# Kernel tuning notes

Measured on AMD Instinct MI355X. Metric: run time of the kernel, lower is better.

Reference implementation:

```python
import jax, jax.numpy as jnp
import numpy as np
import math

E = 8        # num_experts
L2 = 15
L3 = 32
D = 3072     # eval_features_per_perspective
R = 256      # router_features
B = 16384
AUX_ALPHA = 0.01
Z_ALPHA = 0.001


def setup_inputs() -> dict:
    key = jax.random.key(0)
    ks = jax.random.split(key, 12)
    inp = {
        "expert_input": jax.random.uniform(ks[0], (B, D), jnp.float32),
        "router_input": jax.random.normal(ks[1], (R,) , jnp.float32) * 0 + jax.random.normal(ks[1], (B, R), jnp.float32),
        # router init: normal(std=0.01), zero bias (as in _reset_router)
        "router_w": jax.random.normal(ks[2], (E, R), jnp.float32) * 0.01,
        "router_b": jnp.zeros((E,), jnp.float32),
        # FactorizedStackedLinear l1: stacked weight [E*(L2+1), D] + shared factorized [(L2+1), D]
        "l1_w": jax.random.normal(ks[3], (E * (L2 + 1), D), jnp.float32) * (1.0 / math.sqrt(D)),
        "l1_b": jax.random.normal(ks[4], (E * (L2 + 1),), jnp.float32) * 0.01,
        "l1f_w": jax.random.normal(ks[5], (L2 + 1, D), jnp.float32) * (1.0 / math.sqrt(D)),
        "l1f_b": jax.random.normal(ks[6], (L2 + 1,), jnp.float32) * 0.01,
        # StackedLinear l2: [E*L3, 2*L2]
        "l2_w": jax.random.normal(ks[7], (E * L3, 2 * L2), jnp.float32) * (1.0 / math.sqrt(2 * L2)),
        "l2_b": jax.random.normal(ks[8], (E * L3,), jnp.float32) * 0.01,
        # StackedLinear output: [E*1, L3], bias zeroed in __init__
        "out_w": jax.random.normal(ks[9], (E, L3), jnp.float32) * (1.0 / math.sqrt(L3)),
        "out_b": jnp.zeros((E,), jnp.float32),
    }
    return inp


def reference(expert_input, router_input, router_w, router_b,
              l1_w, l1_b, l1f_w, l1f_b, l2_w, l2_b, out_w, out_b):
    # ---- router + straight-through hard gate ----
    gate_logits = router_input @ router_w.T + router_b                      # [B, E]
    gate_probs = jax.nn.softmax(gate_logits, axis=-1)
    expert_indices = jnp.argmax(gate_logits, axis=-1)                       # [B]
    hard_gate = jax.nn.one_hot(expert_indices, E, dtype=gate_probs.dtype)   # [B, E]
    gate = hard_gate + gate_probs - jax.lax.stop_gradient(gate_probs)

    # ---- routing metrics / losses ----
    fraction_routed = hard_gate.mean(axis=0)                                 # [E]
    avg_gate_prob = gate_probs.mean(axis=0)                                  # [E]
    aux_loss = E * jnp.sum(fraction_routed * avg_gate_prob)
    z_loss = jnp.mean(jnp.square(jax.nn.logsumexp(gate_logits, axis=-1)))
    entropy = jnp.mean(-jnp.sum(gate_probs * jnp.log(jnp.clip(gate_probs, 1e-9)), axis=-1))
    normalized_entropy = entropy / jnp.float32(math.log(max(E, 2)))
    top1_prob = jnp.mean(jnp.max(gate_probs, axis=-1))
    router_loss = jnp.float32(AUX_ALPHA) * aux_loss + jnp.float32(Z_ALPHA) * z_loss  # training path

    # ---- l1: FactorizedStackedLinear, dense over all experts (training path) ----
    merged_w = (l1_w + jnp.tile(l1f_w, (E, 1))).reshape(E, L2 + 1, D)        # [E, L2+1, D]
    merged_b = (l1_b + jnp.tile(l1f_b, (E,))).reshape(E, L2 + 1)             # [E, L2+1]
    l1c = jnp.einsum('bi,eoi->beo', expert_input, merged_w) + merged_b[None]  # [B, E, L2+1]
    l1x, l1x_out = l1c[:, :, :L2], l1c[:, :, L2:]                            # [B,E,L2], [B,E,1]
    l1x = jnp.clip(jnp.concatenate([jnp.square(l1x) * (255.0 / 256.0), l1x], axis=2), 0.0, 1.0)  # [B,E,2*L2]

    # ---- l2 + output StackedLinear ----
    w2 = l2_w.reshape(E, L3, 2 * L2)
    l2x = jnp.clip(jnp.einsum('bei,eoi->beo', l1x, w2) + l2_b.reshape(E, L3)[None], 0.0, 1.0)  # [B,E,L3]
    wo = out_w.reshape(E, 1, L3)
    l3x = jnp.einsum('bei,eoi->beo', l2x, wo) + out_b.reshape(E, 1)[None] + l1x_out            # [B,E,1]

    # ---- gated combine ----
    out = jnp.einsum('be,beo->bo', gate, l3x)                                # [B, 1]
    return (out, router_loss, aux_loss, z_loss, fraction_routed, avg_gate_prob,
            normalized_entropy, top1_prob)
```

## Files before the change

kernel.cpp:

```cpp
#include <hip/hip_runtime.h>

constexpr int NB  = 16384;
constexpr int ND  = 3072;
constexpr int NR  = 256;
constexpr int NE  = 8;
constexpr int NO1 = 16;
constexpr int NL2D = 30;
constexpr int NL3 = 32;

constexpr size_t WS_CURSORS = 32;
constexpr size_t WS_OFFPAD  = 128;
constexpr size_t WS_IDX     = 256;
constexpr size_t WS_BUCKET  = WS_IDX + (size_t)NB*4;
constexpr size_t WS_MB      = WS_BUCKET + (size_t)(NB+256)*4;
constexpr size_t WS_MW      = WS_MB + 512;
constexpr size_t WS_BLK_CNT  = WS_MW + (size_t)128*3072*4;
constexpr size_t WS_BLK_SUMP = WS_BLK_CNT + 8192;
constexpr size_t WS_BLK_Z    = WS_BLK_SUMP + 8192;
constexpr size_t WS_BLK_ENT  = WS_BLK_Z + 1024;
constexpr size_t WS_BLK_TOP  = WS_BLK_ENT + 1024;

__device__ __forceinline__ float clamp01(float v) { return fminf(fmaxf(v, 0.0f), 1.0f); }

__device__ __forceinline__ void stage16(const float* g, float* l) {
    __builtin_amdgcn_global_load_lds(
        (const __attribute__((address_space(1))) unsigned int*)g,
        (__attribute__((address_space(3))) unsigned int*)l,
        16, 0, 0);
}

__global__ __launch_bounds__(256) void router_merge_kernel(
    const float* __restrict__ rin, const float* __restrict__ rw,
    const float* __restrict__ rb, int* __restrict__ idx,
    int* __restrict__ blk_cnt, float* __restrict__ blk_sump,
    float* __restrict__ blk_z, float* __restrict__ blk_ent, float* __restrict__ blk_top,
    const float* __restrict__ l1w, const float* __restrict__ l1b,
    const float* __restrict__ l1fw, const float* __restrict__ l1fb,
    float* __restrict__ mw, float* __restrict__ mb)
{
    const int t = threadIdx.x;

    if (blockIdx.x >= 256) {
        const int gid = blockIdx.x - 256;
        const int i4 = gid * 256 + t;
        const float4 a = ((const float4*)l1w)[i4];
        const float4 b = ((const float4*)l1fw)[i4 % (NO1 * ND / 4)];
        float4 r; r.x = a.x + b.x; r.y = a.y + b.y; r.z = a.z + b.z; r.w = a.w + b.w;
        ((float4*)mw)[i4] = r;
        if (gid == 0 && t < NE * NO1) {
            mb[t] = l1b[t] + l1fb[t & (NO1 - 1)];
        }
        return;
    }

    __shared__ float w_s[NE][NR];
    __shared__ float red_f[4][11];
    __shared__ int   red_c[4][8];

    {
        const float4* src = (const float4*)rw;
        float4* dst = (float4*)&w_s[0][0];
        dst[t]       = src[t];
        dst[t + 256] = src[t + 256];
    }
    __syncthreads();

    const int q  = t & 3;
    const int rr = t >> 2;
    const int b  = blockIdx.x * 64 + rr;
    const float* rp = rin + (size_t)b * NR + q * 64;

    float acc[NE];
#pragma unroll
    for (int e = 0; e < NE; ++e) acc[e] = 0.0f;

#pragma unroll
    for (int c = 0; c < 16; ++c) {
        const float4 xv = *(const float4*)(rp + c * 4);
#pragma unroll
        for (int e = 0; e < NE; ++e) {
            const float4 wv = *(const float4*)(&w_s[e][q * 64 + c * 4]);
            acc[e] = fmaf(xv.x, wv.x, acc[e]);
            acc[e] = fmaf(xv.y, wv.y, acc[e]);
            acc[e] = fmaf(xv.z, wv.z, acc[e]);
            acc[e] = fmaf(xv.w, wv.w, acc[e]);
        }
    }
    float lg[NE];
#pragma unroll
    for (int e = 0; e < NE; ++e) {
        float v = acc[e];
        v += __shfl_xor(v, 1);
        v += __shfl_xor(v, 2);
        lg[e] = v + rb[e];
    }

    float m = lg[0]; int am = 0;
#pragma unroll
    for (int e = 1; e < NE; ++e) { if (lg[e] > m) { m = lg[e]; am = e; } }
    float p[NE]; float ssum = 0.0f;
#pragma unroll
    for (int e = 0; e < NE; ++e) { p[e] = __expf(lg[e] - m); ssum += p[e]; }
    const float inv = 1.0f / ssum;
    const float lse = m + __logf(ssum);

    const bool active = (q == 0);
    float sv[11];
    float ent = 0.0f, top = 0.0f;
#pragma unroll
    for (int e = 0; e < NE; ++e) {
        const float pj = p[e] * inv;
        sv[e] = pj;
        ent -= pj * __logf(fmaxf(pj, 1e-9f));
        top = fmaxf(top, pj);
    }
    sv[8] = lse * lse;
    sv[9] = ent;
    sv[10] = top;
    if (!active) {
#pragma unroll
        for (int i = 0; i < 11; ++i) sv[i] = 0.0f;
    }
    if (active) idx[b] = am;

#pragma unroll
    for (int i = 0; i < 11; ++i) {
        float v = sv[i];
        v += __shfl_xor(v, 4);
        v += __shfl_xor(v, 8);
        v += __shfl_xor(v, 16);
        v += __shfl_xor(v, 32);
        sv[i] = v;
    }
    int cnt[NE];
#pragma unroll
    for (int j = 0; j < NE; ++j) {
        unsigned long long mk = __ballot(active && (am == j));
        cnt[j] = __popcll(mk);
    }

    const int wave = t >> 6;
    if ((t & 63) == 0) {
#pragma unroll
        for (int i = 0; i < 11; ++i) red_f[wave][i] = sv[i];
#pragma unroll
        for (int j = 0; j < NE; ++j) red_c[wave][j] = cnt[j];
    }
    __syncthreads();

    const int bid = blockIdx.x;
    if (t < 8) {
        blk_sump[bid * 8 + t] = red_f[0][t] + red_f[1][t] + red_f[2][t] + red_f[3][t];
        blk_cnt [bid * 8 + t] = red_c[0][t] + red_c[1][t] + red_c[2][t] + red_c[3][t];
    } else if (t == 8) {
        blk_z[bid]   = red_f[0][8] + red_f[1][8] + red_f[2][8] + red_f[3][8];
    } else if (t == 9) {
        blk_ent[bid] = red_f[0][9] + red_f[1][9] + red_f[2][9] + red_f[3][9];
    } else if (t == 10) {
        blk_top[bid] = red_f[0][10] + red_f[1][10] + red_f[2][10] + red_f[3][10];
    }
}

__global__ __launch_bounds__(256) void scatter_finalize_kernel(
    const int* __restrict__ blk_cnt, const float* __restrict__ blk_sump,
    const float* __restrict__ blk_z, const float* __restrict__ blk_ent,
    const float* __restrict__ blk_top, const int* __restrict__ idx,
    int* __restrict__ cursors, int* __restrict__ bucket,
    int* __restrict__ offpad, float* __restrict__ out)
{
    const int t = threadIdx.x;

    if (blockIdx.x == 64) {
        __shared__ float ps_s[32][8];
        __shared__ int   pc_s[32][8];
        __shared__ float zet_s[3][4];
        __shared__ float tot_f[8];
        __shared__ int   tot_c[8];
        {
            const int e = t & 7, g = t >> 3;
            float ps = 0.0f; int pc = 0;
#pragma unroll
            for (int k = 0; k < 8; ++k) {
                const int bb = g * 8 + k;
                ps += blk_sump[bb * 8 + e];
                pc += blk_cnt [bb * 8 + e];
            }
            ps_s[g][e] = ps;
            pc_s[g][e] = pc;
        }
        {
            float z = blk_z[t], en = blk_ent[t], tp = blk_top[t];
#pragma unroll
            for (int o = 1; o < 64; o <<= 1) {
                z  += __shfl_xor(z, o);
                en += __shfl_xor(en, o);
                tp += __shfl_xor(tp, o);
            }
            const int wave = t >> 6;
            if ((t & 63) == 0) { zet_s[0][wave] = z; zet_s[1][wave] = en; zet_s[2][wave] = tp; }
        }
        __syncthreads();
        if (t < 8) {
            float s = 0.0f; int c = 0;
            for (int g = 0; g < 32; ++g) { s += ps_s[g][t]; c += pc_s[g][t]; }
            tot_f[t] = s; tot_c[t] = c;
        }
        __syncthreads();
        if (t == 0) {
            int run = 0;
#pragma unroll
            for (int e = 0; e < NE; ++e) {
                offpad[e] = run;
                run += (tot_c[e] + 31) & ~31;
            }
            offpad[NE] = run;

            const float invB = 1.0f / (float)NB;
            float aux = 0.0f;
            float frac[NE], avg[NE];
#pragma unroll
            for (int e = 0; e < NE; ++e) {
                frac[e] = (float)tot_c[e] * invB;
                avg[e]  = tot_f[e] * invB;
                aux += frac[e] * avg[e];
            }
            aux *= (float)NE;
            const float z   = (zet_s[0][0] + zet_s[0][1] + zet_s[0][2] + zet_s[0][3]) * invB;
            const float ent = (zet_s[1][0] + zet_s[1][1] + zet_s[1][2] + zet_s[1][3]) * invB;
            const float top = (zet_s[2][0] + zet_s[2][1] + zet_s[2][2] + zet_s[2][3]) * invB;
            const float rl  = 0.01f * aux + 0.001f * z;

            float* o = out + NB;
            o[0] = rl;
            o[1] = aux;
            o[2] = z;
#pragma unroll
            for (int e = 0; e < NE; ++e) o[3 + e]  = frac[e];
#pragma unroll
            for (int e = 0; e < NE; ++e) o[11 + e] = avg[e];
            o[19] = ent / __logf(8.0f);
            o[20] = top;
        }
        return;
    }

    __shared__ int red_c[4][8];
    __shared__ int offp[8];
    {
        const int4 a = ((const int4*)blk_cnt)[t * 2];
        const int4 bql = ((const int4*)blk_cnt)[t * 2 + 1];
        int v[8] = {a.x, a.y, a.z, a.w, bql.x, bql.y, bql.z, bql.w};
#pragma unroll
        for (int j = 0; j < 8; ++j) {
#pragma unroll
            for (int o = 1; o < 64; o <<= 1) v[j] += __shfl_xor(v[j], o);
        }
        const int wave = t >> 6;
        if ((t & 63) == 0) {
#pragma unroll
            for (int j = 0; j < 8; ++j) red_c[wave][j] = v[j];
        }
    }
    __syncthreads();
    if (t == 0) {
        int run = 0;
#pragma unroll
        for (int e = 0; e < NE; ++e) {
            offp[e] = run;
            run += (red_c[0][e] + red_c[1][e] + red_c[2][e] + red_c[3][e] + 31) & ~31;
        }
    }
    __syncthreads();

    const int b = blockIdx.x * 256 + t;
    const int e = idx[b];
    const int lane = t & 63;
#pragma unroll
    for (int ee = 0; ee < NE; ++ee) {
        unsigned long long mask = __ballot(e == ee);
        if (e == ee) {
            int leader = __ffsll((unsigned long long)mask) - 1;
            int cnt = __popcll(mask);
            int base = 0;
            if (lane == leader) base = atomicAdd(&cursors[ee], cnt);
            base = __shfl(base, leader);
            int pos = base + __popcll(mask & ((1ull << lane) - 1ull));
            bucket[offp[ee] + pos] = b;
        }
    }
}

__global__ __launch_bounds__(256) void moe_main_kernel(
    const float* __restrict__ x, const float* __restrict__ mw,
    const float* __restrict__ mb, const float* __restrict__ l2w,
    const float* __restrict__ l2b, const float* __restrict__ ow,
    const float* __restrict__ ob, const int* __restrict__ bucket,
    const int* __restrict__ offpad, float* __restrict__ out)
{
    __shared__ float x_lds[2][8][128];
    __shared__ int   rows_s[8];
    __shared__ int   expert_s;
    __shared__ float l1c_s[8][16];
    __shared__ float l1x_s[8][30];
    __shared__ float l1c15_s[8];

    const int t = threadIdx.x;
    const int slot0 = blockIdx.x * 8;
    if (t < 8) rows_s[t] = bucket[slot0 + t];
    if (t == 0) {
        int e = 0;
#pragma unroll
        for (int j = 1; j < NE; ++j) if (slot0 >= offpad[j]) e = j;
        expert_s = e;
    }
    __syncthreads();

    const int e    = expert_s;
    const int wid  = t >> 6;
    const int lane = t & 63;
    const int half = lane >> 5;
    const int s    = lane & 31;

    int srow = rows_s[2 * wid + half];
    if (srow < 0) srow = 0;
    const float* xsrc = x + (size_t)srow * ND + s * 4;
    const float* wbase = mw + (size_t)e * NO1 * ND + (size_t)(4 * wid) * ND + s * 4;

    float acc[4][4];
#pragma unroll
    for (int rr = 0; rr < 4; ++rr)
#pragma unroll
        for (int oo = 0; oo < 4; ++oo) acc[rr][oo] = 0.0f;

    stage16(xsrc, &x_lds[0][2 * wid][0]);
    float4 wc0 = *(const float4*)(wbase);
    float4 wc1 = *(const float4*)(wbase + ND);
    float4 wc2 = *(const float4*)(wbase + 2 * ND);
    float4 wc3 = *(const float4*)(wbase + 3 * ND);

    for (int c = 0; c < 24; ++c) {
        const int cur = c & 1;

        float4 wn0, wn1, wn2, wn3;
        if (c + 1 < 24) {
            const float* wk = wbase + (c + 1) * 128;
            wn0 = *(const float4*)(wk);
            wn1 = *(const float4*)(wk + ND);
            wn2 = *(const float4*)(wk + 2 * ND);
            wn3 = *(const float4*)(wk + 3 * ND);
            stage16(xsrc + (c + 1) * 128, &x_lds[cur ^ 1][2 * wid][0]);
            asm volatile("s_waitcnt vmcnt(5)" ::: "memory");
        } else {
            asm volatile("s_waitcnt vmcnt(0)" ::: "memory");
        }
        __builtin_amdgcn_s_barrier();
        __builtin_amdgcn_sched_barrier(0);

        float4 xv[4];
#pragma unroll
        for (int rr = 0; rr < 4; ++rr)
            xv[rr] = *(const float4*)&x_lds[cur][half * 4 + rr][s * 4];

#pragma unroll
        for (int rr = 0; rr < 4; ++rr) {
            acc[rr][0] = fmaf(xv[rr].x, wc0.x, acc[rr][0]);
            acc[rr][0] = fmaf(xv[rr].y, wc0.y, acc[rr][0]);
            acc[rr][0] = fmaf(xv[rr].z, wc0.z, acc[rr][0]);
            acc[rr][0] = fmaf(xv[rr].w, wc0.w, acc[rr][0]);
            acc[rr][1] = fmaf(xv[rr].x, wc1.x, acc[rr][1]);
            acc[rr][1] = fmaf(xv[rr].y, wc1.y, acc[rr][1]);
            acc[rr][1] = fmaf(xv[rr].z, wc1.z, acc[rr][1]);
            acc[rr][1] = fmaf(xv[rr].w, wc1.w, acc[rr][1]);
            acc[rr][2] = fmaf(xv[rr].x, wc2.x, acc[rr][2]);
            acc[rr][2] = fmaf(xv[rr].y, wc2.y, acc[rr][2]);
            acc[rr][2] = fmaf(xv[rr].z, wc2.z, acc[rr][2]);
            acc[rr][2] = fmaf(xv[rr].w, wc2.w, acc[rr][2]);
            acc[rr][3] = fmaf(xv[rr].x, wc3.x, acc[rr][3]);
            acc[rr][3] = fmaf(xv[rr].y, wc3.y, acc[rr][3]);
            acc[rr][3] = fmaf(xv[rr].z, wc3.z, acc[rr][3]);
            acc[rr][3] = fmaf(xv[rr].w, wc3.w, acc[rr][3]);
        }

        asm volatile("s_waitcnt lgkmcnt(0)" ::: "memory");
        __builtin_amdgcn_s_barrier();

        if (c + 1 < 24) { wc0 = wn0; wc1 = wn1; wc2 = wn2; wc3 = wn3; }
    }

#pragma unroll
    for (int rr = 0; rr < 4; ++rr)
#pragma unroll
        for (int oo = 0; oo < 4; ++oo) {
            float a = acc[rr][oo];
            a += __shfl_xor(a, 1);
            a += __shfl_xor(a, 2);
            a += __shfl_xor(a, 4);
            a += __shfl_xor(a, 8);
            a += __shfl_xor(a, 16);
            acc[rr][oo] = a;
        }
    if (s == 0) {
#pragma unroll
        for (int rr = 0; rr < 4; ++rr)
#pragma unroll
            for (int oo = 0; oo < 4; ++oo)
                l1c_s[half * 4 + rr][4 * wid + oo] = acc[rr][oo];
    }
    __syncthreads();

    const int r = t >> 5;
    const int q = t & 31;
    const int rowb = rows_s[r];

    if (q < 16) {
        const int o = q;
        float v = l1c_s[r][o] + mb[e * NO1 + o];
        if (o < 15) {
            l1x_s[r][o]      = clamp01(v * v * (255.0f / 256.0f));
            l1x_s[r][o + 15] = clamp01(v);
        } else {
            l1c15_s[r] = v;
        }
    }
    __syncthreads();

    float a2 = l2b[e * NL3 + q];
    const float* w2r = l2w + (size_t)e * NL3 * NL2D + q * NL2D;
#pragma unroll
    for (int i = 0; i < NL2D; ++i) a2 = fmaf(l1x_s[r][i], w2r[i], a2);
    a2 = clamp01(a2);
    float pacc = a2 * ow[e * NL3 + q];
    pacc += __shfl_xor(pacc, 1);
    pacc += __shfl_xor(pacc, 2);
    pacc += __shfl_xor(pacc, 4);
    pacc += __shfl_xor(pacc, 8);
    pacc += __shfl_xor(pacc, 16);

    if (q == 0 && rowb >= 0) {
        out[rowb] = pacc + ob[e] + l1c15_s[r];
    }
}

extern "C" void kernel_launch(void* const* d_in, const int* in_sizes, int n_in,
                              void* d_out, int out_size, void* d_ws, size_t ws_size,
                              hipStream_t stream)
{
    const float* x    = (const float*)d_in[0];
    const float* rin  = (const float*)d_in[1];
    const float* rw   = (const float*)d_in[2];
    const float* rb   = (const float*)d_in[3];
    const float* l1w  = (const float*)d_in[4];
    const float* l1b  = (const float*)d_in[5];
    const float* l1fw = (const float*)d_in[6];
    const float* l1fb = (const float*)d_in[7];
    const float* l2w  = (const float*)d_in[8];
    const float* l2b  = (const float*)d_in[9];
    const float* ow   = (const float*)d_in[10];
    const float* ob   = (const float*)d_in[11];
    float* out = (float*)d_out;

    char* ws = (char*)d_ws;
    int*   cursors = (int*)(ws + WS_CURSORS);
    int*   offpad  = (int*)(ws + WS_OFFPAD);
    int*   idx     = (int*)(ws + WS_IDX);
    int*   bucket  = (int*)(ws + WS_BUCKET);
    float* mb      = (float*)(ws + WS_MB);
    float* mw      = (float*)(ws + WS_MW);
    int*   blk_cnt  = (int*)(ws + WS_BLK_CNT);
    float* blk_sump = (float*)(ws + WS_BLK_SUMP);
    float* blk_z    = (float*)(ws + WS_BLK_Z);
    float* blk_ent  = (float*)(ws + WS_BLK_ENT);
    float* blk_top  = (float*)(ws + WS_BLK_TOP);

    hipMemsetAsync(ws, 0, 256, stream);
    hipMemsetAsync(ws + WS_BUCKET, 0xFF, (size_t)(NB + 256) * 4, stream);

    router_merge_kernel<<<640, 256, 0, stream>>>(rin, rw, rb, idx, blk_cnt, blk_sump,
                                                 blk_z, blk_ent, blk_top,
                                                 l1w, l1b, l1fw, l1fb, mw, mb);
    scatter_finalize_kernel<<<65, 256, 0, stream>>>(blk_cnt, blk_sump, blk_z, blk_ent,
                                                    blk_top, idx, cursors, bucket,
                                                    offpad, out);
    moe_main_kernel<<<(NB + 256) / 8, 256, 0, stream>>>(x, mw, mb, l2w, l2b, ow, ob,
                                                        bucket, offpad, out);
}
```

Measured before the change: 99.07 us.

## Split L1 reduction over K into two segments with separate tail kernel

The fused MoE kernel is split in two. The L1 GEMV kernel now runs over a 2D grid, where each block handles half of the 3072-wide K dimension and writes partial 16-wide results to a workspace slab. A new tail kernel sums the two partials, adds the bias and runs the L2/output layers per row. The aim is more parallelism and shorter per-block serial loops, so the GPU is better filled and latency is hidden. The cost is an extra kernel launch and a round trip of the partials through global memory.

```diff
diff --git a/kernel.cpp b/kernel.cpp
--- a/kernel.cpp
+++ b/kernel.cpp
@@ -7,6 +7,7 @@
 constexpr int NO1 = 16;
 constexpr int NL2D = 30;
 constexpr int NL3 = 32;
+constexpr int KSEG = 1536;
 
 constexpr size_t WS_CURSORS = 32;
 constexpr size_t WS_OFFPAD  = 128;
@@ -19,6 +20,7 @@
 constexpr size_t WS_BLK_Z    = WS_BLK_SUMP + 8192;
 constexpr size_t WS_BLK_ENT  = WS_BLK_Z + 1024;
 constexpr size_t WS_BLK_TOP  = WS_BLK_ENT + 1024;
+constexpr size_t WS_SLAB     = WS_BLK_TOP + 1024;
 
 __device__ __forceinline__ float clamp01(float v) { return fminf(fmaxf(v, 0.0f), 1.0f); }
 
@@ -290,22 +292,18 @@
     }
 }
 
-__global__ __launch_bounds__(256) void moe_main_kernel(
+__global__ __launch_bounds__(256) void moe_l1_kernel(
     const float* __restrict__ x, const float* __restrict__ mw,
-    const float* __restrict__ mb, const float* __restrict__ l2w,
-    const float* __restrict__ l2b, const float* __restrict__ ow,
-    const float* __restrict__ ob, const int* __restrict__ bucket,
-    const int* __restrict__ offpad, float* __restrict__ out)
+    const int* __restrict__ bucket, const int* __restrict__ offpad,
+    float* __restrict__ slab)
 {
     __shared__ float x_lds[2][8][128];
     __shared__ int   rows_s[8];
     __shared__ int   expert_s;
-    __shared__ float l1c_s[8][16];
-    __shared__ float l1x_s[8][30];
-    __shared__ float l1c15_s[8];
 
     const int t = threadIdx.x;
     const int slot0 = blockIdx.x * 8;
+    const int seg = blockIdx.y;
     if (t < 8) rows_s[t] = bucket[slot0 + t];
     if (t == 0) {
         int e = 0;
@@ -323,8 +321,8 @@
 
     int srow = rows_s[2 * wid + half];
     if (srow < 0) srow = 0;
-    const float* xsrc = x + (size_t)srow * ND + s * 4;
-    const float* wbase = mw + (size_t)e * NO1 * ND + (size_t)(4 * wid) * ND + s * 4;
+    const float* xsrc = x + (size_t)srow * ND + seg * KSEG + s * 4;
+    const float* wbase = mw + (size_t)e * NO1 * ND + (size_t)(4 * wid) * ND + seg * KSEG + s * 4;
 
     float acc[4][4];
 #pragma unroll
@@ -338,11 +336,11 @@
     float4 wc2 = *(const float4*)(wbase + 2 * ND);
     float4 wc3 = *(const float4*)(wbase + 3 * ND);
 
-    for (int c = 0; c < 24; ++c) {
+    for (int c = 0; c < 12; ++c) {
         const int cur = c & 1;
 
         float4 wn0, wn1, wn2, wn3;
-        if (c + 1 < 24) {
+        if (c + 1 < 12) {
             const float* wk = wbase + (c + 1) * 128;
             wn0 = *(const float4*)(wk);
             wn1 = *(const float4*)(wk + ND);
@@ -384,7 +382,7 @@
         asm volatile("s_waitcnt lgkmcnt(0)" ::: "memory");
         __builtin_amdgcn_s_barrier();
 
-        if (c + 1 < 24) { wc0 = wn0; wc1 = wn1; wc2 = wn2; wc3 = wn3; }
+        if (c + 1 < 12) { wc0 = wn0; wc1 = wn1; wc2 = wn2; wc3 = wn3; }
     }
 
 #pragma unroll
@@ -399,45 +397,69 @@
             a += __shfl_xor(a, 16);
             acc[rr][oo] = a;
         }
+
     if (s == 0) {
 #pragma unroll
-        for (int rr = 0; rr < 4; ++rr)
-#pragma unroll
-            for (int oo = 0; oo < 4; ++oo)
-                l1c_s[half * 4 + rr][4 * wid + oo] = acc[rr][oo];
-    }
-    __syncthreads();
-
-    const int r = t >> 5;
-    const int q = t & 31;
-    const int rowb = rows_s[r];
-
-    if (q < 16) {
-        const int o = q;
-        float v = l1c_s[r][o] + mb[e * NO1 + o];
-        if (o < 15) {
-            l1x_s[r][o]      = clamp01(v * v * (255.0f / 256.0f));
-            l1x_s[r][o + 15] = clamp01(v);
+        for (int rr = 0; rr < 4; ++rr) {
+            const int rowb = rows_s[half * 4 + rr];
+            if (rowb >= 0) {
+                float4 v;
+                v.x = acc[rr][0]; v.y = acc[rr][1]; v.z = acc[rr][2]; v.w = acc[rr][3];
+                *(float4*)&slab[((size_t)seg * NB + rowb) * NO1 + 4 * wid] = v;
+            }
+        }
+    }
+}
+
+__global__ __launch_bounds__(256) void moe_tail_kernel(
+    const int* __restrict__ idx, const float* __restrict__ mb,
+    const float* __restrict__ l2w, const float* __restrict__ l2b,
+    const float* __restrict__ ow, const float* __restrict__ ob,
+    const float* __restrict__ slab, float* __restrict__ out)
+{
+    __shared__ float l1x_s[16][30];
+    __shared__ float l1c15_s[16];
+    __shared__ int   e_s[16];
+
+    const int t = threadIdx.x;
+    const int r = t >> 4;
+    const int q = t & 15;
+    const int row = blockIdx.x * 16 + r;
+
+    const int e = idx[row];
+    if (q == 0) e_s[r] = e;
+
+    {
+        const float v0 = slab[(size_t)row * NO1 + q];
+        const float v1 = slab[((size_t)NB + row) * NO1 + q];
+        const float v = v0 + v1 + mb[e * NO1 + q];
+        if (q < 15) {
+            l1x_s[r][q]      = clamp01(v * v * (255.0f / 256.0f));
+            l1x_s[r][q + 15] = clamp01(v);
         } else {
             l1c15_s[r] = v;
         }
     }
     __syncthreads();
 
-    float a2 = l2b[e * NL3 + q];
-    const float* w2r = l2w + (size_t)e * NL3 * NL2D + q * NL2D;
-#pragma unroll
-    for (int i = 0; i < NL2D; ++i) a2 = fmaf(l1x_s[r][i], w2r[i], a2);
-    a2 = clamp01(a2);
-    float pacc = a2 * ow[e * NL3 + q];
+    float pacc = 0.0f;
+#pragma unroll
+    for (int oo = 0; oo < 2; ++oo) {
+        const int o2 = q + oo * 16;
+        float a2 = l2b[e * NL3 + o2];
+        const float* w2r = l2w + (size_t)e * NL3 * NL2D + o2 * NL2D;
+#pragma unroll
+        for (int i = 0; i < NL2D; ++i) a2 = fmaf(l1x_s[r][i], w2r[i], a2);
+        a2 = clamp01(a2);
+        pacc = fmaf(a2, ow[e * NL3 + o2], pacc);
+    }
     pacc += __shfl_xor(pacc, 1);
     pacc += __shfl_xor(pacc, 2);
     pacc += __shfl_xor(pacc, 4);
     pacc += __shfl_xor(pacc, 8);
-    pacc += __shfl_xor(pacc, 16);
-
-    if (q == 0 && rowb >= 0) {
-        out[rowb] = pacc + ob[e] + l1c15_s[r];
+
+    if (q == 0) {
+        out[row] = pacc + ob[e] + l1c15_s[r];
     }
 }
 
@@ -471,6 +493,7 @@
     float* blk_z    = (float*)(ws + WS_BLK_Z);
     float* blk_ent  = (float*)(ws + WS_BLK_ENT);
     float* blk_top  = (float*)(ws + WS_BLK_TOP);
+    float* slab     = (float*)(ws + WS_SLAB);
 
     hipMemsetAsync(ws, 0, 256, stream);
     hipMemsetAsync(ws + WS_BUCKET, 0xFF, (size_t)(NB + 256) * 4, stream);
@@ -481,6 +504,6 @@
     scatter_finalize_kernel<<<65, 256, 0, stream>>>(blk_cnt, blk_sump, blk_z, blk_ent,
                                                     blk_top, idx, cursors, bucket,
                                                     offpad, out);
-    moe_main_kernel<<<(NB + 256) / 8, 256, 0, stream>>>(x, mw, mb, l2w, l2b, ow, ob,
-                                                        bucket, offpad, out);
+    moe_l1_kernel<<<dim3((NB + 256) / 8, 2), 256, 0, stream>>>(x, mw, bucket, offpad, slab);
+    moe_tail_kernel<<<NB / 16, 256, 0, stream>>>(idx, mb, l2w, l2b, ow, ob, slab, out);
 }
```

After: 110.8 us. +11.9%, slower.
